# Optimization experiments

Hardware: AMD Instinct MI355X
Metric: run time of the kernel (lower is better)

## Reference

```python
import jax, jax.numpy as jnp
import numpy as np

N = 50000       # population nodes
E = 1_600_000   # edges per edge type
F_IN = 2000     # flattened individual-graph embedding (100*20)
D = 20          # hidden channels per TransformerConv head (heads=1)
NEG_SLOPE = 0.01
BN_EPS = 1e-5


def setup_inputs() -> dict:
    key = jax.random.key(0)
    ks = jax.random.split(key, 24)
    features = jax.random.normal(ks[0], (N, F_IN), jnp.float32)
    same_index = jax.random.randint(ks[1], (2, E), 0, N, dtype=jnp.int64)
    diff_index = jax.random.randint(ks[2], (2, E), 0, N, dtype=jnp.int64)
    s0 = 1.0 / np.sqrt(F_IN)
    s1 = 1.0 / np.sqrt(D)
    # layer 0 conv params, stacked over the 2 edge types (same, diff)
    W0q = jax.random.normal(ks[3], (2, F_IN, D), jnp.float32) * s0
    W0k = jax.random.normal(ks[4], (2, F_IN, D), jnp.float32) * s0
    W0v = jax.random.normal(ks[5], (2, F_IN, D), jnp.float32) * s0
    W0s = jax.random.normal(ks[6], (2, F_IN, D), jnp.float32) * s0
    b0q = jnp.zeros((2, D)); b0k = jnp.zeros((2, D))
    b0v = jnp.zeros((2, D)); b0s = jnp.zeros((2, D))
    # layers 1..3 conv params: [layer, edge_type, D, D]
    Wq = jax.random.normal(ks[7], (3, 2, D, D), jnp.float32) * s1
    Wk = jax.random.normal(ks[8], (3, 2, D, D), jnp.float32) * s1
    Wv = jax.random.normal(ks[9], (3, 2, D, D), jnp.float32) * s1
    Ws = jax.random.normal(ks[10], (3, 2, D, D), jnp.float32) * s1
    bq = jnp.zeros((3, 2, D)); bk = jnp.zeros((3, 2, D))
    bv = jnp.zeros((3, 2, D)); bs = jnp.zeros((3, 2, D))
    w1 = jnp.full((4,), 0.8, jnp.float32)
    w2 = jnp.full((4,), 0.2, jnp.float32)
    bn_gamma = jnp.ones((4, D), jnp.float32)
    bn_beta = jnp.zeros((4, D), jnp.float32)
    Wout = jax.random.normal(ks[11], (4 * D, 2), jnp.float32) / np.sqrt(4 * D)
    bout = jnp.zeros((2,), jnp.float32)
    return dict(features=features, same_index=same_index, diff_index=diff_index,
                W0q=W0q, b0q=b0q, W0k=W0k, b0k=b0k, W0v=W0v, b0v=b0v, W0s=W0s, b0s=b0s,
                Wq=Wq, bq=bq, Wk=Wk, bk=bk, Wv=Wv, bv=bv, Ws=Ws, bs=bs,
                w1=w1, w2=w2, bn_gamma=bn_gamma, bn_beta=bn_beta, Wout=Wout, bout=bout)


def _tconv(x, edge_index, Wq, bq, Wk, bk, Wv, bv, Ws, bs):
    """PyG TransformerConv, heads=1, concat=True, root_weight=True, no edge_attr."""
    src, dst = edge_index[0], edge_index[1]
    q = x @ Wq + bq   # [N, D]
    k = x @ Wk + bk
    v = x @ Wv + bv
    logits = jnp.einsum('ed,ed->e', q[dst], k[src]) / jnp.sqrt(jnp.float32(D))  # [E]
    m = jax.ops.segment_max(logits, dst, num_segments=N)
    m = jnp.where(jnp.isfinite(m), m, jnp.float32(0.0))  # nodes with no in-edges
    e = jnp.exp(logits - m[dst])
    z = jax.ops.segment_sum(e, dst, num_segments=N)
    alpha = e / (z[dst] + 1e-16)  # PyG softmax epsilon
    agg = jax.ops.segment_sum(alpha[:, None] * v[src], dst, num_segments=N)  # [N, D]
    return agg + x @ Ws + bs  # skip (root) connection


def _bn(x, gamma, beta):
    mu = x.mean(axis=0)
    var = x.var(axis=0)
    return (x - mu) * jax.lax.rsqrt(var + BN_EPS) * gamma + beta


def reference(features, same_index, diff_index,
              W0q, b0q, W0k, b0k, W0v, b0v, W0s, b0s,
              Wq, bq, Wk, bk, Wv, bv, Ws, bs,
              w1, w2, bn_gamma, bn_beta, Wout, bout):
    x = features
    fcs = []
    for l in range(4):
        if l == 0:
            p_same = (W0q[0], b0q[0], W0k[0], b0k[0], W0v[0], b0v[0], W0s[0], b0s[0])
            p_diff = (W0q[1], b0q[1], W0k[1], b0k[1], W0v[1], b0v[1], W0s[1], b0s[1])
        else:
            i = l - 1
            p_same = (Wq[i, 0], bq[i, 0], Wk[i, 0], bk[i, 0], Wv[i, 0], bv[i, 0], Ws[i, 0], bs[i, 0])
            p_diff = (Wq[i, 1], bq[i, 1], Wk[i, 1], bk[i, 1], Wv[i, 1], bv[i, 1], Ws[i, 1], bs[i, 1])
        x1 = _tconv(x, same_index, *p_same)
        x2 = _tconv(x, diff_index, *p_diff)
        t = w1[l] + w2[l]
        x = (w1[l] / t) * x1 + (w2[l] / t) * x2
        x = _bn(x, bn_gamma[l], bn_beta[l])
        x = jax.nn.leaky_relu(x, NEG_SLOPE)
        fcs.append(x)
    fc = jnp.concatenate(fcs, axis=-1)  # [N, 80]
    return fc @ Wout + bout  # [N, 2]
```

## Files before the change

kernel.cpp:

```cpp
#include <hip/hip_runtime.h>
#include <math.h>

#define N_NODES 50000
#define E_EDGES 1600000
#define F_IN    2000
#define D       20
#define NCOL    160
#define KPAD    2016
#define NBNP    64

#define INV_SQRT_D 0.22360679774997896f

typedef __bf16 bf16x8 __attribute__((ext_vector_type(8)));
typedef __bf16 bf16x4 __attribute__((ext_vector_type(4)));
typedef float  f32x4  __attribute__((ext_vector_type(4)));


__global__ void pack_kernel(
    const float* __restrict__ W0q, const float* __restrict__ W0k,
    const float* __restrict__ W0v, const float* __restrict__ W0s,
    const float* __restrict__ b0q, const float* __restrict__ b0k,
    const float* __restrict__ b0v, const float* __restrict__ b0s,
    const float* __restrict__ Wq,  const float* __restrict__ Wk,
    const float* __restrict__ Wv,  const float* __restrict__ Ws_,
    const float* __restrict__ bq,  const float* __restrict__ bk,
    const float* __restrict__ bv,  const float* __restrict__ bs_,
    __bf16* __restrict__ B0, float* __restrict__ bias0,
    float* __restrict__ WL, float* __restrict__ biasL,
    float* __restrict__ bnp, int* __restrict__ deg)
{
  long idx = (long)blockIdx.x * blockDim.x + threadIdx.x;
  if (idx < (long)NCOL*KPAD) {
    int col = (int)(idx / KPAD), k = (int)(idx % KPAD);
    int et = col / 80, r = col % 80, mat = r / 20, d = r % 20;
    const float* w = (mat==0)?W0q:(mat==1)?W0s:(mat==2)?W0k:W0v;
    float v = (k < F_IN) ? w[((size_t)et*F_IN + k)*D + d] : 0.f;
    B0[idx] = (__bf16)v;
    return;
  }
  idx -= (long)NCOL*KPAD;
  if (idx < 160) {
    int col = (int)idx;
    int et = col / 80, r = col % 80, mat = r / 20, d = r % 20;
    const float* b = (mat==0)?b0q:(mat==1)?b0s:(mat==2)?b0k:b0v;
    bias0[col] = b[et*D + d];
    return;
  }
  idx -= 160;
  if (idx < 9600) {
    int l = (int)(idx / 3200), rem = (int)(idx % 3200);
    int k = rem / NCOL, col = rem % NCOL;
    int et = col / 80, r = col % 80, mat = r / 20, d = r % 20;
    const float* w = (mat==0)?Wq:(mat==1)?Ws_:(mat==2)?Wk:Wv;
    WL[idx] = w[(((size_t)l*2 + et)*D + k)*D + d];
    return;
  }
  idx -= 9600;
  if (idx < 480) {
    int l = (int)(idx / NCOL), col = (int)(idx % NCOL);
    int et = col / 80, r = col % 80, mat = r / 20, d = r % 20;
    const float* b = (mat==0)?bq:(mat==1)?bs_:(mat==2)?bk:bv;
    biasL[idx] = b[(l*2 + et)*D + d];
    return;
  }
  idx -= 480;
  if (idx < 4*NBNP*40) { bnp[idx] = 0.f; return; }
  idx -= 4*NBNP*40;
  if (idx < 2*N_NODES) { deg[idx] = 0; return; }
}

__global__ void hist_kernel(const int* __restrict__ same, const int* __restrict__ diff,
                            int* __restrict__ deg)
{
  long i = (long)blockIdx.x * blockDim.x + threadIdx.x;
  if (i >= 2L*E_EDGES) return;
  int et = (i >= E_EDGES) ? 1 : 0;
  long e = i - (long)et*E_EDGES;
  const int* ix = et ? diff : same;
  int dst = ix[E_EDGES + e];
  atomicAdd(&deg[(size_t)et*N_NODES + dst], 1);
}

__global__ void scan_kernel(const int* __restrict__ deg,
                            int* __restrict__ rowptr0, int* __restrict__ rowptr1,
                            int* __restrict__ next0, int* __restrict__ next1)
{
  const int et = blockIdx.x;
  const int* dg = deg + (size_t)et*N_NODES;
  int* rp = et ? rowptr1 : rowptr0;
  int* np = et ? next1 : next0;
  __shared__ int part[1024];
  const int t = threadIdx.x;
  const int per = (N_NODES + 1023) / 1024;
  const int b = t * per;
  const int e = (b + per < N_NODES) ? (b + per) : N_NODES;
  int s = 0;
  for (int i = b; i < e; i++) s += dg[i];
  part[t] = s;
  __syncthreads();
  for (int o = 1; o < 1024; o <<= 1) {
    int v = (t >= o) ? part[t-o] : 0;
    __syncthreads();
    part[t] += v;
    __syncthreads();
  }
  int run = (t == 0) ? 0 : part[t-1];
  for (int i = b; i < e; i++) {
    rp[i] = run; np[i] = run;
    run += dg[i];
  }
  if (t == 0) rp[N_NODES] = part[1023];
}

#define SC_EPT 16
#define SC_CHUNK (256*SC_EPT)
__global__ void scatter_kernel(const int* __restrict__ same, const int* __restrict__ diff,
                               int* __restrict__ next0, int* __restrict__ next1,
                               int* __restrict__ adj0, int* __restrict__ adj1)
{
  const int part  = blockIdx.x & 7;
  const int chunk = blockIdx.x >> 3;
  const int lo = part * (N_NODES/8);
  const int hi = lo + (N_NODES/8);
  const long i0 = (long)chunk * SC_CHUNK + threadIdx.x;
#pragma unroll
  for (int it = 0; it < SC_EPT; ++it) {
    long i = i0 + (long)it*256;
    if (i >= 2L*E_EDGES) break;
    int et = (i >= E_EDGES) ? 1 : 0;
    long e = i - (long)et*E_EDGES;
    const int* ix = et ? diff : same;
    int dst = ix[E_EDGES + e];
    if (dst >= lo && dst < hi) {
      int src = ix[e];
      int* np  = et ? next1 : next0;
      int* adj = et ? adj1  : adj0;
      int pos = atomicAdd(&np[dst], 1);
      adj[pos] = src;
    }
  }
}

__launch_bounds__(512)
__global__ void gemm0_mfma(const float* __restrict__ A,
                           const __bf16* __restrict__ Bt,
                           const float* __restrict__ bias,
                           __bf16* __restrict__ QS,
                           __bf16* __restrict__ KV0, __bf16* __restrict__ KV1)
{
  __shared__ __bf16 as[128*32];
  const int t    = threadIdx.x;
  const int lane = t & 63;
  const int wid  = t >> 6;
  const int wr   = wid >> 1;
  const int wc   = wid & 1;
  const int rb0  = blockIdx.x * 128;

  const int srow = t >> 2;
  const int skc  = (t & 3) * 8;
  const int arow = rb0 + srow;
  const float* aptr = A + (size_t)arow * F_IN;

  const int lrow = lane & 15;
  const int lkb  = (lane >> 4) * 8;

  f32x4 acc[2][5];
#pragma unroll
  for (int i = 0; i < 2; i++)
#pragma unroll
    for (int j = 0; j < 5; j++) acc[i][j] = (f32x4){0.f,0.f,0.f,0.f};

  float4 p0, p1;
  auto loadA = [&](int k0) {
    int k = k0 + skc;
    if (arow < N_NODES) {
      if (k + 8 <= F_IN) {
        p0 = *(const float4*)(aptr + k);
        p1 = *(const float4*)(aptr + k + 4);
      } else {
        float tmp[8];
#pragma unroll
        for (int i = 0; i < 8; i++) tmp[i] = (k + i < F_IN) ? aptr[k + i] : 0.f;
        p0 = make_float4(tmp[0],tmp[1],tmp[2],tmp[3]);
        p1 = make_float4(tmp[4],tmp[5],tmp[6],tmp[7]);
      }
    } else {
      p0 = make_float4(0,0,0,0); p1 = p0;
    }
  };

  loadA(0);
  for (int s = 0; s < 63; s++) {
    bf16x8 h;
    h[0]=(__bf16)p0.x; h[1]=(__bf16)p0.y; h[2]=(__bf16)p0.z; h[3]=(__bf16)p0.w;
    h[4]=(__bf16)p1.x; h[5]=(__bf16)p1.y; h[6]=(__bf16)p1.z; h[7]=(__bf16)p1.w;
    *(bf16x8*)&as[srow*32 + skc] = h;
    __syncthreads();
    if (s + 1 < 63) loadA((s + 1) * 32);

    bf16x8 af[2];
#pragma unroll
    for (int rf = 0; rf < 2; rf++)
      af[rf] = *(bf16x8*)&as[(wr*32 + rf*16 + lrow)*32 + lkb];
    bf16x8 bfr[5];
#pragma unroll
    for (int cf = 0; cf < 5; cf++)
      bfr[cf] = *(const bf16x8*)(Bt + (size_t)(wc*80 + cf*16 + lrow)*KPAD + s*32 + lkb);
#pragma unroll
    for (int rf = 0; rf < 2; rf++)
#pragma unroll
      for (int cf = 0; cf < 5; cf++)
        acc[rf][cf] = __builtin_amdgcn_mfma_f32_16x16x32_bf16(af[rf], bfr[cf], acc[rf][cf], 0, 0, 0);
    __syncthreads();
  }

#pragma unroll
  for (int rf = 0; rf < 2; rf++) {
#pragma unroll
    for (int cf = 0; cf < 5; cf++) {
      int col = wc*80 + cf*16 + lrow;
      int et = col / 80, r = col % 80, mat = r / 20, d = r % 20;
      float bv = bias[col];
      __bf16* kvp = et ? KV1 : KV0;
#pragma unroll
      for (int j = 0; j < 4; j++) {
        int row = rb0 + wr*32 + rf*16 + (lane >> 4)*4 + j;
        if (row < N_NODES) {
          __bf16 val = (__bf16)(acc[rf][cf][j] + bv);
          if (mat < 2) QS[(size_t)row*80 + et*40 + mat*20 + d] = val;
          else         kvp[(size_t)row*64 + (mat-2)*20 + d]   = val;
        }
      }
    }
  }
}

__launch_bounds__(256)
__global__ void proj_small_kernel(const float* __restrict__ xp, const float* __restrict__ bnl,
                                  const float* __restrict__ gam, const float* __restrict__ bet,
                                  const float* __restrict__ W, const float* __restrict__ bias,
                                  __bf16* __restrict__ QS,
                                  __bf16* __restrict__ KV0, __bf16* __restrict__ KV1)
{
  __shared__ float ws[20*160];
  __shared__ float xs[16*20];
  __shared__ float Ac[20], Bc[20];
  const int t = threadIdx.x;
  const int n0 = blockIdx.x * 16;
#pragma unroll
  for (int i = 0; i < 13; i++) {
    int idx = t + i*256;
    if (idx < 3200) ws[idx] = W[idx];
  }
  if (t < 20) {
    float s1 = 0.f, s2 = 0.f;
    for (int s = 0; s < NBNP; s++) { s1 += bnl[s*40 + t]; s2 += bnl[s*40 + 20 + t]; }
    float mu  = s1 * (1.f/N_NODES);
    float var = s2 * (1.f/N_NODES) - mu*mu;
    float a = rsqrtf(var + 1e-5f) * gam[t];
    Ac[t] = a; Bc[t] = bet[t] - mu*a;
  }
  __syncthreads();
#pragma unroll
  for (int i = 0; i < 2; i++) {
    int idx = t + i*256;
    if (idx < 320) {
      int nl = idx / 20, k = idx % 20;
      int n = n0 + nl;
      float x = (n < N_NODES) ? xp[(size_t)n*D + k] : 0.f;
      float y = x*Ac[k] + Bc[k];
      xs[idx] = (y > 0.f) ? y : 0.01f*y;
    }
  }
  __syncthreads();
#pragma unroll
  for (int i = 0; i < 10; i++) {
    int idx = t + i*256;
    int nl = idx / NCOL, col = idx % NCOL;
    int n = n0 + nl;
    if (n < N_NODES) {
      float acc = bias[col];
#pragma unroll
      for (int k = 0; k < 20; k++) acc += xs[nl*20 + k] * ws[k*NCOL + col];
      int et = col / 80, r = col % 80, mat = r / 20, d = r % 20;
      __bf16 val = (__bf16)acc;
      if (mat < 2) QS[(size_t)n*80 + et*40 + mat*20 + d] = val;
      else         (et ? KV1 : KV0)[(size_t)n*64 + (mat-2)*20 + d] = val;
    }
  }
}

__launch_bounds__(256)
__global__ void attn_fused(const int* __restrict__ rp0, const int* __restrict__ adj0,
                           const int* __restrict__ rp1, const int* __restrict__ adj1,
                           const __bf16* __restrict__ QS,
                           const __bf16* __restrict__ KV0, const __bf16* __restrict__ KV1,
                           const float* __restrict__ w1, const float* __restrict__ w2, int l,
                           float* __restrict__ xpre, float* __restrict__ bnp)
{
  __shared__ float xnode[4][20];
  const int t    = threadIdx.x;
  const int wv   = t >> 6;
  const int lane = t & 63;
  const int half = lane >> 5;
  const int sl   = lane & 31;
  const int node = blockIdx.x*4 + wv;

  const int* rowptr = half ? rp1 : rp0;
  const int* adj    = half ? adj1 : adj0;
  const __bf16* kvb = half ? KV1 : KV0;
  const __bf16* rq  = QS + (size_t)node*80 + half*40;

  float qf[20];
  {
    bf16x8 q0 = *(const bf16x8*)(rq);
    bf16x8 q1 = *(const bf16x8*)(rq + 8);
    bf16x4 q2 = *(const bf16x4*)(rq + 16);
#pragma unroll
    for (int i = 0; i < 8; i++) { qf[i] = (float)q0[i]; qf[8+i] = (float)q1[i]; }
#pragma unroll
    for (int i = 0; i < 4; i++) qf[16+i] = (float)q2[i];
  }

  const int beg = rowptr[node], end = rowptr[node+1];
  float z = 0.f;
  float S[20];
#pragma unroll
  for (int d = 0; d < 20; d++) S[d] = 0.f;

  for (int i = beg + sl; i < end; i += 32) {
    const int src = adj[i];
    const __bf16* kv = kvb + (size_t)src*64;
    bf16x8 a0 = *(const bf16x8*)(kv);
    bf16x8 a1 = *(const bf16x8*)(kv + 8);
    bf16x8 a2 = *(const bf16x8*)(kv + 16);
    bf16x8 a3 = *(const bf16x8*)(kv + 24);
    bf16x8 a4 = *(const bf16x8*)(kv + 32);
    float d0 = 0.f;
#pragma unroll
    for (int j = 0; j < 8; j++) d0 += qf[j]     * (float)a0[j];
#pragma unroll
    for (int j = 0; j < 8; j++) d0 += qf[8 + j] * (float)a1[j];
#pragma unroll
    for (int j = 0; j < 4; j++) d0 += qf[16 + j]* (float)a2[j];
    const float w0 = __expf(fminf(d0*INV_SQRT_D, 80.f));
    z += w0;
#pragma unroll
    for (int d = 0; d < 4; d++) S[d]     += w0*(float)a2[4+d];
#pragma unroll
    for (int d = 0; d < 8; d++) S[4+d]   += w0*(float)a3[d];
#pragma unroll
    for (int d = 0; d < 8; d++) S[12+d]  += w0*(float)a4[d];
  }

#pragma unroll
  for (int o = 16; o >= 1; o >>= 1) {
    z += __shfl_xor(z, o, 64);
#pragma unroll
    for (int d = 0; d < 20; d++) S[d] += __shfl_xor(S[d], o, 64);
  }

  const float inv = (z > 0.f) ? 1.f/z : 0.f;
  float outv[20];
  {
    bf16x4 s0 = *(const bf16x4*)(rq + 20);
    bf16x8 s1 = *(const bf16x8*)(rq + 24);
    bf16x8 s2 = *(const bf16x8*)(rq + 32);
#pragma unroll
    for (int i = 0; i < 4; i++) outv[i] = S[i]*inv + (float)s0[i];
#pragma unroll
    for (int i = 0; i < 8; i++) { outv[4+i]  = S[4+i]*inv  + (float)s1[i];
                                  outv[12+i] = S[12+i]*inv + (float)s2[i]; }
  }

  const float wa = w1[l], wb = w2[l];
  const float c0 = wa/(wa+wb), c1 = wb/(wa+wb);
  const float cme = half ? c1 : c0;
  const float cot = half ? c0 : c1;
  float x[20];
#pragma unroll
  for (int d = 0; d < 20; d++) {
    float o2 = __shfl_xor(outv[d], 32, 64);
    x[d] = cme*outv[d] + cot*o2;
  }

  if (lane == 0) {
    float* xo = xpre + (size_t)node*D;
#pragma unroll
    for (int j = 0; j < 5; j++) {
      float4 o4 = make_float4(x[4*j], x[4*j+1], x[4*j+2], x[4*j+3]);
      *(float4*)(xo + 4*j) = o4;
    }
#pragma unroll
    for (int d = 0; d < 20; d++) xnode[wv][d] = x[d];
  }
  __syncthreads();

  if (t < 20) {
    float s1 = xnode[0][t] + xnode[1][t] + xnode[2][t] + xnode[3][t];
    float s2 = xnode[0][t]*xnode[0][t] + xnode[1][t]*xnode[1][t]
             + xnode[2][t]*xnode[2][t] + xnode[3][t]*xnode[3][t];
    float* slot = bnp + (blockIdx.x & (NBNP-1))*40;
    atomicAdd(&slot[t], s1);
    atomicAdd(&slot[20 + t], s2);
  }
}

__launch_bounds__(256)
__global__ void final_kernel(const float* __restrict__ xpre4, const float* __restrict__ bnp,
                             const float* __restrict__ gam, const float* __restrict__ bet,
                             const float* __restrict__ Wout, const float* __restrict__ bout,
                             float* __restrict__ out)
{
  __shared__ float Ac[80], Bc[80], wlds[160];
  const int t = threadIdx.x;
  if (t < 80) {
    int l = t / 20, d = t % 20;
    const float* b = bnp + l*(NBNP*40);
    float s1 = 0.f, s2 = 0.f;
    for (int s = 0; s < NBNP; s++) { s1 += b[s*40 + d]; s2 += b[s*40 + 20 + d]; }
    float mu  = s1 * (1.f/N_NODES);
    float var = s2 * (1.f/N_NODES) - mu*mu;
    float a = rsqrtf(var + 1e-5f) * gam[t];
    Ac[t] = a; Bc[t] = bet[t] - mu*a;
  }
  if (t < 160) wlds[t] = Wout[t];
  __syncthreads();

  const int n = blockIdx.x*256 + t;
  if (n >= N_NODES) return;
  float a0 = bout[0], a1 = bout[1];
#pragma unroll
  for (int l = 0; l < 4; l++) {
    const float* base = xpre4 + (size_t)l*N_NODES*D + (size_t)n*D;
#pragma unroll
    for (int d = 0; d < D; d++) {
      int idx = l*20 + d;
      float y = base[d]*Ac[idx] + Bc[idx];
      y = (y > 0.f) ? y : 0.01f*y;
      a0 += y * wlds[idx*2 + 0];
      a1 += y * wlds[idx*2 + 1];
    }
  }
  out[n*2+0] = a0;
  out[n*2+1] = a1;
}

extern "C" void kernel_launch(void* const* d_in, const int* in_sizes, int n_in,
                              void* d_out, int out_size, void* d_ws, size_t ws_size,
                              hipStream_t stream)
{
  const float* feat = (const float*)d_in[0];
  const int*   same = (const int*)d_in[1];
  const int*   diff = (const int*)d_in[2];
  const float* W0q = (const float*)d_in[3];
  const float* b0q = (const float*)d_in[4];
  const float* W0k = (const float*)d_in[5];
  const float* b0k = (const float*)d_in[6];
  const float* W0v = (const float*)d_in[7];
  const float* b0v = (const float*)d_in[8];
  const float* W0s = (const float*)d_in[9];
  const float* b0s = (const float*)d_in[10];
  const float* Wq  = (const float*)d_in[11];
  const float* bq  = (const float*)d_in[12];
  const float* Wk  = (const float*)d_in[13];
  const float* bk  = (const float*)d_in[14];
  const float* Wv  = (const float*)d_in[15];
  const float* bv  = (const float*)d_in[16];
  const float* Ws_ = (const float*)d_in[17];
  const float* bs_ = (const float*)d_in[18];
  const float* w1  = (const float*)d_in[19];
  const float* w2  = (const float*)d_in[20];
  const float* gamma = (const float*)d_in[21];
  const float* beta  = (const float*)d_in[22];
  const float* Wout  = (const float*)d_in[23];
  const float* bout  = (const float*)d_in[24];

  float* wsf  = (float*)d_ws;
  __bf16*  QS    = (__bf16*)wsf;
  __bf16*  KV0   = (__bf16*)(wsf + 2000000);
  __bf16*  KV1   = (__bf16*)(wsf + 3600000);
  float*   XPRE4 = wsf + 5200000;
  __bf16*  B0bf  = (__bf16*)(wsf + 9200000);
  float*   BIAS0 = wsf + 9361280;
  float*   WL    = wsf + 9361440;
  float*   BIASL = wsf + 9371040;
  float*   BNP   = wsf + 9371520;
  int*     ib    = (int*)(wsf + 9381760);
  int* DEG  = ib;
  int* RP0  = ib + 100000;
  int* RP1  = ib + 150004;
  int* NX0  = ib + 200008;
  int* NX1  = ib + 250008;
  int* ADJ0 = ib + 300008;
  int* ADJ1 = ib + 1900008;

  const int packN = NCOL*KPAD + 160 + 9600 + 480 + 4*NBNP*40 + 2*N_NODES;
  pack_kernel<<<(packN + 255)/256, 256, 0, stream>>>(
      W0q, W0k, W0v, W0s, b0q, b0k, b0v, b0s,
      Wq, Wk, Wv, Ws_, bq, bk, bv, bs_,
      B0bf, BIAS0, WL, BIASL, BNP, DEG);

  hist_kernel<<<(2*E_EDGES + 255)/256, 256, 0, stream>>>(same, diff, DEG);
  scan_kernel<<<2, 1024, 0, stream>>>(DEG, RP0, RP1, NX0, NX1);
  {
    const long nchunk = (2L*E_EDGES + SC_CHUNK - 1) / SC_CHUNK;
    scatter_kernel<<<(int)(nchunk*8), 256, 0, stream>>>(same, diff, NX0, NX1, ADJ0, ADJ1);
  }

  for (int l = 0; l < 4; l++) {
    if (l == 0)
      gemm0_mfma<<<(N_NODES + 127)/128, 512, 0, stream>>>(feat, B0bf, BIAS0, QS, KV0, KV1);
    else
      proj_small_kernel<<<(N_NODES + 15)/16, 256, 0, stream>>>(
          XPRE4 + (size_t)(l-1)*N_NODES*D, BNP + (l-1)*(NBNP*40),
          gamma + (l-1)*D, beta + (l-1)*D,
          WL + (size_t)(l-1)*3200, BIASL + (size_t)(l-1)*160, QS, KV0, KV1);

    attn_fused<<<N_NODES/4, 256, 0, stream>>>(
        RP0, ADJ0, RP1, ADJ1, QS, KV0, KV1, w1, w2, l,
        XPRE4 + (size_t)l*N_NODES*D, BNP + l*(NBNP*40));
  }

  final_kernel<<<(N_NODES + 255)/256, 256, 0, stream>>>(
      XPRE4, BNP, gamma, beta, Wout, bout, (float*)d_out);
}
```

Baseline: 986.9 us.

## Fuse GEMM, projection, attention and final layers into one cooperative persistent kernel

Replaces the per-layer sequence of gemm0, proj_small, attn_fused and final kernels with a single cooperative persistent kernel that uses grid.sync between stages. The goal is to remove launch overhead and the inter-kernel drains. The layer-0 GEMM now uses 64-row tiles with 256 threads. BN partial sums are atomically accumulated per node-lane instead of per block via shared memory, and hist_kernel is partitioned by destination range like scatter. The trade-offs are grid-wide barrier costs, reduced occupancy from a fixed grid size, and more atomic traffic on the BN slots.

```diff
diff --git a/kernel.cpp b/kernel.cpp
--- a/kernel.cpp
+++ b/kernel.cpp
@@ -1,5 +1,8 @@
 #include <hip/hip_runtime.h>
+#include <hip/hip_cooperative_groups.h>
 #include <math.h>
+
+namespace cg = cooperative_groups;
 
 #define N_NODES 50000
 #define E_EDGES 1600000
@@ -14,7 +17,6 @@
 typedef __bf16 bf16x8 __attribute__((ext_vector_type(8)));
 typedef __bf16 bf16x4 __attribute__((ext_vector_type(4)));
 typedef float  f32x4  __attribute__((ext_vector_type(4)));
-
 
 __global__ void pack_kernel(
     const float* __restrict__ W0q, const float* __restrict__ W0k,
@@ -69,16 +71,28 @@
   if (idx < 2*N_NODES) { deg[idx] = 0; return; }
 }
 
+#define SC_EPT 16
+#define SC_CHUNK (256*SC_EPT)
+
 __global__ void hist_kernel(const int* __restrict__ same, const int* __restrict__ diff,
                             int* __restrict__ deg)
 {
-  long i = (long)blockIdx.x * blockDim.x + threadIdx.x;
-  if (i >= 2L*E_EDGES) return;
-  int et = (i >= E_EDGES) ? 1 : 0;
-  long e = i - (long)et*E_EDGES;
-  const int* ix = et ? diff : same;
-  int dst = ix[E_EDGES + e];
-  atomicAdd(&deg[(size_t)et*N_NODES + dst], 1);
+  const int part  = blockIdx.x & 7;
+  const int chunk = blockIdx.x >> 3;
+  const int lo = part * (N_NODES/8);
+  const int hi = lo + (N_NODES/8);
+  const long i0 = (long)chunk * SC_CHUNK + threadIdx.x;
+#pragma unroll
+  for (int it = 0; it < SC_EPT; ++it) {
+    long i = i0 + (long)it*256;
+    if (i >= 2L*E_EDGES) break;
+    int et = (i >= E_EDGES) ? 1 : 0;
+    long e = i - (long)et*E_EDGES;
+    const int* ix = et ? diff : same;
+    int dst = ix[E_EDGES + e];
+    if (dst >= lo && dst < hi)
+      atomicAdd(&deg[(size_t)et*N_NODES + dst], 1);
+  }
 }
 
 __global__ void scan_kernel(const int* __restrict__ deg,
@@ -112,8 +126,6 @@
   if (t == 0) rp[N_NODES] = part[1023];
 }
 
-#define SC_EPT 16
-#define SC_CHUNK (256*SC_EPT)
 __global__ void scatter_kernel(const int* __restrict__ same, const int* __restrict__ diff,
                                int* __restrict__ next0, int* __restrict__ next1,
                                int* __restrict__ adj0, int* __restrict__ adj1)
@@ -141,309 +153,313 @@
   }
 }
 
-__launch_bounds__(512)
-__global__ void gemm0_mfma(const float* __restrict__ A,
-                           const __bf16* __restrict__ Bt,
-                           const float* __restrict__ bias,
-                           __bf16* __restrict__ QS,
-                           __bf16* __restrict__ KV0, __bf16* __restrict__ KV1)
+struct MegaP {
+  const float* feat; const __bf16* B0; const float* bias0;
+  const float* WL; const float* biasL;
+  const float* w1; const float* w2; const float* gamma; const float* beta;
+  const float* Wout; const float* bout;
+  const int* rp0; const int* adj0; const int* rp1; const int* adj1;
+  __bf16* QS; __bf16* KV0; __bf16* KV1;
+  float* xpre4; float* bnp; float* out;
+};
+
+__launch_bounds__(256, 4)
+__global__ void mega_kernel(MegaP P)
 {
-  __shared__ __bf16 as[128*32];
+  cg::grid_group grid = cg::this_grid();
+  __shared__ __align__(16) char smem[14336];
   const int t    = threadIdx.x;
+  const int nblk = gridDim.x;
   const int lane = t & 63;
-  const int wid  = t >> 6;
-  const int wr   = wid >> 1;
-  const int wc   = wid & 1;
-  const int rb0  = blockIdx.x * 128;
-
-  const int srow = t >> 2;
-  const int skc  = (t & 3) * 8;
-  const int arow = rb0 + srow;
-  const float* aptr = A + (size_t)arow * F_IN;
-
-  const int lrow = lane & 15;
-  const int lkb  = (lane >> 4) * 8;
-
-  f32x4 acc[2][5];
-#pragma unroll
-  for (int i = 0; i < 2; i++)
-#pragma unroll
-    for (int j = 0; j < 5; j++) acc[i][j] = (f32x4){0.f,0.f,0.f,0.f};
-
-  float4 p0, p1;
-  auto loadA = [&](int k0) {
-    int k = k0 + skc;
-    if (arow < N_NODES) {
-      if (k + 8 <= F_IN) {
-        p0 = *(const float4*)(aptr + k);
-        p1 = *(const float4*)(aptr + k + 4);
-      } else {
-        float tmp[8];
-#pragma unroll
-        for (int i = 0; i < 8; i++) tmp[i] = (k + i < F_IN) ? aptr[k + i] : 0.f;
-        p0 = make_float4(tmp[0],tmp[1],tmp[2],tmp[3]);
-        p1 = make_float4(tmp[4],tmp[5],tmp[6],tmp[7]);
-      }
-    } else {
-      p0 = make_float4(0,0,0,0); p1 = p0;
+  const int wv   = t >> 6;
+
+  {
+    __bf16* as = (__bf16*)smem;
+    const int wr   = wv >> 1;
+    const int wc   = wv & 1;
+    const int srow = t >> 2;
+    const int skc  = (t & 3) * 8;
+    const int lrow = lane & 15;
+    const int lkb  = (lane >> 4) * 8;
+
+    for (int tile = blockIdx.x; tile < 782; tile += nblk) {
+      const int rb0  = tile * 64;
+      const int arow = rb0 + srow;
+      const float* aptr = P.feat + (size_t)arow * F_IN;
+
+      f32x4 acc[2][5];
+#pragma unroll
+      for (int i = 0; i < 2; i++)
+#pragma unroll
+        for (int j = 0; j < 5; j++) acc[i][j] = (f32x4){0.f,0.f,0.f,0.f};
+
+      float4 p0, p1;
+      auto loadA = [&](int k0) {
+        int k = k0 + skc;
+        if (arow < N_NODES) {
+          p0 = *(const float4*)(aptr + k);
+          p1 = *(const float4*)(aptr + k + 4);
+        } else {
+          p0 = make_float4(0,0,0,0); p1 = p0;
+        }
+      };
+
+      loadA(0);
+      for (int s = 0; s < 63; s++) {
+        bf16x8 h;
+        h[0]=(__bf16)p0.x; h[1]=(__bf16)p0.y; h[2]=(__bf16)p0.z; h[3]=(__bf16)p0.w;
+        h[4]=(__bf16)p1.x; h[5]=(__bf16)p1.y; h[6]=(__bf16)p1.z; h[7]=(__bf16)p1.w;
+        __syncthreads();
+        *(bf16x8*)&as[srow*32 + skc] = h;
+        __syncthreads();
+        if (s + 1 < 63) loadA((s + 1) * 32);
+
+        bf16x8 af[2];
+#pragma unroll
+        for (int rf = 0; rf < 2; rf++)
+          af[rf] = *(bf16x8*)&as[(wr*32 + rf*16 + lrow)*32 + lkb];
+        bf16x8 bfr[5];
+#pragma unroll
+        for (int cf = 0; cf < 5; cf++)
+          bfr[cf] = *(const bf16x8*)(P.B0 + (size_t)(wc*80 + cf*16 + lrow)*KPAD + s*32 + lkb);
+#pragma unroll
+        for (int rf = 0; rf < 2; rf++)
+#pragma unroll
+          for (int cf = 0; cf < 5; cf++)
+            acc[rf][cf] = __builtin_amdgcn_mfma_f32_16x16x32_bf16(af[rf], bfr[cf], acc[rf][cf], 0, 0, 0);
+      }
+
+#pragma unroll
+      for (int rf = 0; rf < 2; rf++) {
+#pragma unroll
+        for (int cf = 0; cf < 5; cf++) {
+          int col = wc*80 + cf*16 + lrow;
+          int et = col / 80, r = col % 80, mat = r / 20, d = r % 20;
+          float bv = P.bias0[col];
+          __bf16* kvp = et ? P.KV1 : P.KV0;
+#pragma unroll
+          for (int j = 0; j < 4; j++) {
+            int row = rb0 + wr*32 + rf*16 + (lane >> 4)*4 + j;
+            if (row < N_NODES) {
+              __bf16 val = (__bf16)(acc[rf][cf][j] + bv);
+              if (mat < 2) P.QS[(size_t)row*80 + et*40 + mat*20 + d] = val;
+              else         kvp[(size_t)row*64 + (mat-2)*20 + d]     = val;
+            }
+          }
+        }
+      }
     }
-  };
-
-  loadA(0);
-  for (int s = 0; s < 63; s++) {
-    bf16x8 h;
-    h[0]=(__bf16)p0.x; h[1]=(__bf16)p0.y; h[2]=(__bf16)p0.z; h[3]=(__bf16)p0.w;
-    h[4]=(__bf16)p1.x; h[5]=(__bf16)p1.y; h[6]=(__bf16)p1.z; h[7]=(__bf16)p1.w;
-    *(bf16x8*)&as[srow*32 + skc] = h;
+  }
+  grid.sync();
+
+  for (int l = 0; l < 4; ++l) {
+    if (l > 0) {
+      float* ws = (float*)smem;
+      float* xs = (float*)smem + 3200;
+      float* Ac = (float*)smem + 3520;
+      float* Bc = (float*)smem + 3540;
+      const float* bnl  = P.bnp + (size_t)(l-1)*(NBNP*40);
+      const float* W    = P.WL + (size_t)(l-1)*3200;
+      const float* bias = P.biasL + (size_t)(l-1)*160;
+      const float* xp   = P.xpre4 + (size_t)(l-1)*N_NODES*D;
+
+      __syncthreads();
+#pragma unroll
+      for (int i = 0; i < 13; i++) {
+        int idx = t + i*256;
+        if (idx < 3200) ws[idx] = W[idx];
+      }
+      if (t < 20) {
+        float s1 = 0.f, s2 = 0.f;
+        for (int s = 0; s < NBNP; s++) { s1 += bnl[s*40 + t]; s2 += bnl[s*40 + 20 + t]; }
+        float mu  = s1 * (1.f/N_NODES);
+        float var = s2 * (1.f/N_NODES) - mu*mu;
+        float a = rsqrtf(var + 1e-5f) * P.gamma[(l-1)*D + t];
+        Ac[t] = a; Bc[t] = P.beta[(l-1)*D + t] - mu*a;
+      }
+      __syncthreads();
+
+      for (int tile = blockIdx.x; tile < 3125; tile += nblk) {
+        const int n0 = tile * 16;
+        __syncthreads();
+#pragma unroll
+        for (int i = 0; i < 2; i++) {
+          int idx = t + i*256;
+          if (idx < 320) {
+            int nl = idx / 20, k = idx % 20;
+            int n = n0 + nl;
+            float x = (n < N_NODES) ? xp[(size_t)n*D + k] : 0.f;
+            float y = x*Ac[k] + Bc[k];
+            xs[idx] = (y > 0.f) ? y : 0.01f*y;
+          }
+        }
+        __syncthreads();
+#pragma unroll
+        for (int i = 0; i < 10; i++) {
+          int idx = t + i*256;
+          int nl = idx / NCOL, col = idx % NCOL;
+          int n = n0 + nl;
+          if (n < N_NODES) {
+            float acc = bias[col];
+#pragma unroll
+            for (int k = 0; k < 20; k++) acc += xs[nl*20 + k] * ws[k*NCOL + col];
+            int et = col / 80, r = col % 80, mat = r / 20, d = r % 20;
+            __bf16 val = (__bf16)acc;
+            if (mat < 2) P.QS[(size_t)n*80 + et*40 + mat*20 + d] = val;
+            else         (et ? P.KV1 : P.KV0)[(size_t)n*64 + (mat-2)*20 + d] = val;
+          }
+        }
+      }
+      grid.sync();
+    }
+
+    {
+      const int half = lane >> 5;
+      const int sl   = lane & 31;
+      const int* rowptr = half ? P.rp1 : P.rp0;
+      const int* adj    = half ? P.adj1 : P.adj0;
+      const __bf16* kvb = half ? P.KV1 : P.KV0;
+      const float wa = P.w1[l], wb = P.w2[l];
+      const float c0 = wa/(wa+wb), c1 = wb/(wa+wb);
+      const float cme = half ? c1 : c0;
+      const float cot = half ? c0 : c1;
+      float* xpre = P.xpre4 + (size_t)l*N_NODES*D;
+      float* bnpl = P.bnp + (size_t)l*(NBNP*40);
+
+      for (int g = blockIdx.x; g < 12500; g += nblk) {
+        const int node = g*4 + wv;
+        const __bf16* rq = P.QS + (size_t)node*80 + half*40;
+
+        float qf[20];
+        {
+          bf16x8 q0 = *(const bf16x8*)(rq);
+          bf16x8 q1 = *(const bf16x8*)(rq + 8);
+          bf16x4 q2 = *(const bf16x4*)(rq + 16);
+#pragma unroll
+          for (int i = 0; i < 8; i++) { qf[i] = (float)q0[i]; qf[8+i] = (float)q1[i]; }
+#pragma unroll
+          for (int i = 0; i < 4; i++) qf[16+i] = (float)q2[i];
+        }
+
+        const int beg = rowptr[node], end = rowptr[node+1];
+        float z = 0.f;
+        float S[20];
+#pragma unroll
+        for (int d = 0; d < 20; d++) S[d] = 0.f;
+
+        for (int i = beg + sl; i < end; i += 32) {
+          const int src = adj[i];
+          const __bf16* kv = kvb + (size_t)src*64;
+          bf16x8 a0 = *(const bf16x8*)(kv);
+          bf16x8 a1 = *(const bf16x8*)(kv + 8);
+          bf16x8 a2 = *(const bf16x8*)(kv + 16);
+          bf16x8 a3 = *(const bf16x8*)(kv + 24);
+          bf16x8 a4 = *(const bf16x8*)(kv + 32);
+          float d0 = 0.f;
+#pragma unroll
+          for (int j = 0; j < 8; j++) d0 += qf[j]     * (float)a0[j];
+#pragma unroll
+          for (int j = 0; j < 8; j++) d0 += qf[8 + j] * (float)a1[j];
+#pragma unroll
+          for (int j = 0; j < 4; j++) d0 += qf[16 + j]* (float)a2[j];
+          const float w0 = __expf(fminf(d0*INV_SQRT_D, 80.f));
+          z += w0;
+#pragma unroll
+          for (int d = 0; d < 4; d++) S[d]     += w0*(float)a2[4+d];
+#pragma unroll
+          for (int d = 0; d < 8; d++) S[4+d]   += w0*(float)a3[d];
+#pragma unroll
+          for (int d = 0; d < 8; d++) S[12+d]  += w0*(float)a4[d];
+        }
+
+#pragma unroll
+        for (int o = 16; o >= 1; o >>= 1) {
+          z += __shfl_xor(z, o, 64);
+#pragma unroll
+          for (int d = 0; d < 20; d++) S[d] += __shfl_xor(S[d], o, 64);
+        }
+
+        const float inv = (z > 0.f) ? 1.f/z : 0.f;
+        float outv[20];
+        {
+          bf16x4 s0 = *(const bf16x4*)(rq + 20);
+          bf16x8 s1 = *(const bf16x8*)(rq + 24);
+          bf16x8 s2 = *(const bf16x8*)(rq + 32);
+#pragma unroll
+          for (int i2 = 0; i2 < 4; i2++) outv[i2] = S[i2]*inv + (float)s0[i2];
+#pragma unroll
+          for (int i2 = 0; i2 < 8; i2++) { outv[4+i2]  = S[4+i2]*inv  + (float)s1[i2];
+                                           outv[12+i2] = S[12+i2]*inv + (float)s2[i2]; }
+        }
+
+        float x[20];
+#pragma unroll
+        for (int d = 0; d < 20; d++) {
+          float o2 = __shfl_xor(outv[d], 32, 64);
+          x[d] = cme*outv[d] + cot*o2;
+        }
+
+        if (lane == 0) {
+          float* xo = xpre + (size_t)node*D;
+#pragma unroll
+          for (int j = 0; j < 5; j++) {
+            float4 o4 = make_float4(x[4*j], x[4*j+1], x[4*j+2], x[4*j+3]);
+            *(float4*)(xo + 4*j) = o4;
+          }
+        }
+
+        float v = x[0];
+#pragma unroll
+        for (int d = 1; d < 20; d++) v = (sl == d) ? x[d] : v;
+        if (sl < 20) {
+          float* slot = bnpl + (size_t)(node & (NBNP-1))*40;
+          if (half == 0) atomicAdd(&slot[sl], v);
+          else           atomicAdd(&slot[20 + sl], v*v);
+        }
+      }
+    }
+    grid.sync();
+  }
+
+  {
+    float* Ac   = (float*)smem;
+    float* Bc   = (float*)smem + 80;
+    float* wlds = (float*)smem + 160;
     __syncthreads();
-    if (s + 1 < 63) loadA((s + 1) * 32);
-
-    bf16x8 af[2];
-#pragma unroll
-    for (int rf = 0; rf < 2; rf++)
-      af[rf] = *(bf16x8*)&as[(wr*32 + rf*16 + lrow)*32 + lkb];
-    bf16x8 bfr[5];
-#pragma unroll
-    for (int cf = 0; cf < 5; cf++)
-      bfr[cf] = *(const bf16x8*)(Bt + (size_t)(wc*80 + cf*16 + lrow)*KPAD + s*32 + lkb);
-#pragma unroll
-    for (int rf = 0; rf < 2; rf++)
-#pragma unroll
-      for (int cf = 0; cf < 5; cf++)
-        acc[rf][cf] = __builtin_amdgcn_mfma_f32_16x16x32_bf16(af[rf], bfr[cf], acc[rf][cf], 0, 0, 0);
+    if (t < 80) {
+      int l = t / 20, d = t % 20;
+      const float* b = P.bnp + (size_t)l*(NBNP*40);
+      float s1 = 0.f, s2 = 0.f;
+      for (int s = 0; s < NBNP; s++) { s1 += b[s*40 + d]; s2 += b[s*40 + 20 + d]; }
+      float mu  = s1 * (1.f/N_NODES);
+      float var = s2 * (1.f/N_NODES) - mu*mu;
+      float a = rsqrtf(var + 1e-5f) * P.gamma[t];
+      Ac[t] = a; Bc[t] = P.beta[t] - mu*a;
+    }
+    if (t < 160) wlds[t] = P.Wout[t];
     __syncthreads();
-  }
-
-#pragma unroll
-  for (int rf = 0; rf < 2; rf++) {
-#pragma unroll
-    for (int cf = 0; cf < 5; cf++) {
-      int col = wc*80 + cf*16 + lrow;
-      int et = col / 80, r = col % 80, mat = r / 20, d = r % 20;
-      float bv = bias[col];
-      __bf16* kvp = et ? KV1 : KV0;
-#pragma unroll
-      for (int j = 0; j < 4; j++) {
-        int row = rb0 + wr*32 + rf*16 + (lane >> 4)*4 + j;
-        if (row < N_NODES) {
-          __bf16 val = (__bf16)(acc[rf][cf][j] + bv);
-          if (mat < 2) QS[(size_t)row*80 + et*40 + mat*20 + d] = val;
-          else         kvp[(size_t)row*64 + (mat-2)*20 + d]   = val;
-        }
-      }
+
+    const float b0 = P.bout[0], b1 = P.bout[1];
+    for (int tile = blockIdx.x; tile < 196; tile += nblk) {
+      const int n = tile*256 + t;
+      if (n >= N_NODES) continue;
+      float a0 = b0, a1 = b1;
+#pragma unroll
+      for (int l = 0; l < 4; l++) {
+        const float* base = P.xpre4 + (size_t)l*N_NODES*D + (size_t)n*D;
+#pragma unroll
+        for (int d = 0; d < D; d++) {
+          int idx = l*20 + d;
+          float y = base[d]*Ac[idx] + Bc[idx];
+          y = (y > 0.f) ? y : 0.01f*y;
+          a0 += y * wlds[idx*2 + 0];
+          a1 += y * wlds[idx*2 + 1];
+        }
+      }
+      P.out[n*2+0] = a0;
+      P.out[n*2+1] = a1;
     }
   }
-}
-
-__launch_bounds__(256)
-__global__ void proj_small_kernel(const float* __restrict__ xp, const float* __restrict__ bnl,
-                                  const float* __restrict__ gam, const float* __restrict__ bet,
-                                  const float* __restrict__ W, const float* __restrict__ bias,
-                                  __bf16* __restrict__ QS,
-                                  __bf16* __restrict__ KV0, __bf16* __restrict__ KV1)
-{
-  __shared__ float ws[20*160];
-  __shared__ float xs[16*20];
-  __shared__ float Ac[20], Bc[20];
-  const int t = threadIdx.x;
-  const int n0 = blockIdx.x * 16;
-#pragma unroll
-  for (int i = 0; i < 13; i++) {
-    int idx = t + i*256;
-    if (idx < 3200) ws[idx] = W[idx];
-  }
-  if (t < 20) {
-    float s1 = 0.f, s2 = 0.f;
-    for (int s = 0; s < NBNP; s++) { s1 += bnl[s*40 + t]; s2 += bnl[s*40 + 20 + t]; }
-    float mu  = s1 * (1.f/N_NODES);
-    float var = s2 * (1.f/N_NODES) - mu*mu;
-    float a = rsqrtf(var + 1e-5f) * gam[t];
-    Ac[t] = a; Bc[t] = bet[t] - mu*a;
-  }
-  __syncthreads();
-#pragma unroll
-  for (int i = 0; i < 2; i++) {
-    int idx = t + i*256;
-    if (idx < 320) {
-      int nl = idx / 20, k = idx % 20;
-      int n = n0 + nl;
-      float x = (n < N_NODES) ? xp[(size_t)n*D + k] : 0.f;
-      float y = x*Ac[k] + Bc[k];
-      xs[idx] = (y > 0.f) ? y : 0.01f*y;
-    }
-  }
-  __syncthreads();
-#pragma unroll
-  for (int i = 0; i < 10; i++) {
-    int idx = t + i*256;
-    int nl = idx / NCOL, col = idx % NCOL;
-    int n = n0 + nl;
-    if (n < N_NODES) {
-      float acc = bias[col];
-#pragma unroll
-      for (int k = 0; k < 20; k++) acc += xs[nl*20 + k] * ws[k*NCOL + col];
-      int et = col / 80, r = col % 80, mat = r / 20, d = r % 20;
-      __bf16 val = (__bf16)acc;
-      if (mat < 2) QS[(size_t)n*80 + et*40 + mat*20 + d] = val;
-      else         (et ? KV1 : KV0)[(size_t)n*64 + (mat-2)*20 + d] = val;
-    }
-  }
-}
-
-__launch_bounds__(256)
-__global__ void attn_fused(const int* __restrict__ rp0, const int* __restrict__ adj0,
-                           const int* __restrict__ rp1, const int* __restrict__ adj1,
-                           const __bf16* __restrict__ QS,
-                           const __bf16* __restrict__ KV0, const __bf16* __restrict__ KV1,
-                           const float* __restrict__ w1, const float* __restrict__ w2, int l,
-                           float* __restrict__ xpre, float* __restrict__ bnp)
-{
-  __shared__ float xnode[4][20];
-  const int t    = threadIdx.x;
-  const int wv   = t >> 6;
-  const int lane = t & 63;
-  const int half = lane >> 5;
-  const int sl   = lane & 31;
-  const int node = blockIdx.x*4 + wv;
-
-  const int* rowptr = half ? rp1 : rp0;
-  const int* adj    = half ? adj1 : adj0;
-  const __bf16* kvb = half ? KV1 : KV0;
-  const __bf16* rq  = QS + (size_t)node*80 + half*40;
-
-  float qf[20];
-  {
-    bf16x8 q0 = *(const bf16x8*)(rq);
-    bf16x8 q1 = *(const bf16x8*)(rq + 8);
-    bf16x4 q2 = *(const bf16x4*)(rq + 16);
-#pragma unroll
-    for (int i = 0; i < 8; i++) { qf[i] = (float)q0[i]; qf[8+i] = (float)q1[i]; }
-#pragma unroll
-    for (int i = 0; i < 4; i++) qf[16+i] = (float)q2[i];
-  }
-
-  const int beg = rowptr[node], end = rowptr[node+1];
-  float z = 0.f;
-  float S[20];
-#pragma unroll
-  for (int d = 0; d < 20; d++) S[d] = 0.f;
-
-  for (int i = beg + sl; i < end; i += 32) {
-    const int src = adj[i];
-    const __bf16* kv = kvb + (size_t)src*64;
-    bf16x8 a0 = *(const bf16x8*)(kv);
-    bf16x8 a1 = *(const bf16x8*)(kv + 8);
-    bf16x8 a2 = *(const bf16x8*)(kv + 16);
-    bf16x8 a3 = *(const bf16x8*)(kv + 24);
-    bf16x8 a4 = *(const bf16x8*)(kv + 32);
-    float d0 = 0.f;
-#pragma unroll
-    for (int j = 0; j < 8; j++) d0 += qf[j]     * (float)a0[j];
-#pragma unroll
-    for (int j = 0; j < 8; j++) d0 += qf[8 + j] * (float)a1[j];
-#pragma unroll
-    for (int j = 0; j < 4; j++) d0 += qf[16 + j]* (float)a2[j];
-    const float w0 = __expf(fminf(d0*INV_SQRT_D, 80.f));
-    z += w0;
-#pragma unroll
-    for (int d = 0; d < 4; d++) S[d]     += w0*(float)a2[4+d];
-#pragma unroll
-    for (int d = 0; d < 8; d++) S[4+d]   += w0*(float)a3[d];
-#pragma unroll
-    for (int d = 0; d < 8; d++) S[12+d]  += w0*(float)a4[d];
-  }
-
-#pragma unroll
-  for (int o = 16; o >= 1; o >>= 1) {
-    z += __shfl_xor(z, o, 64);
-#pragma unroll
-    for (int d = 0; d < 20; d++) S[d] += __shfl_xor(S[d], o, 64);
-  }
-
-  const float inv = (z > 0.f) ? 1.f/z : 0.f;
-  float outv[20];
-  {
-    bf16x4 s0 = *(const bf16x4*)(rq + 20);
-    bf16x8 s1 = *(const bf16x8*)(rq + 24);
-    bf16x8 s2 = *(const bf16x8*)(rq + 32);
-#pragma unroll
-    for (int i = 0; i < 4; i++) outv[i] = S[i]*inv + (float)s0[i];
-#pragma unroll
-    for (int i = 0; i < 8; i++) { outv[4+i]  = S[4+i]*inv  + (float)s1[i];
-                                  outv[12+i] = S[12+i]*inv + (float)s2[i]; }
-  }
-
-  const float wa = w1[l], wb = w2[l];
-  const float c0 = wa/(wa+wb), c1 = wb/(wa+wb);
-  const float cme = half ? c1 : c0;
-  const float cot = half ? c0 : c1;
-  float x[20];
-#pragma unroll
-  for (int d = 0; d < 20; d++) {
-    float o2 = __shfl_xor(outv[d], 32, 64);
-    x[d] = cme*outv[d] + cot*o2;
-  }
-
-  if (lane == 0) {
-    float* xo = xpre + (size_t)node*D;
-#pragma unroll
-    for (int j = 0; j < 5; j++) {
-      float4 o4 = make_float4(x[4*j], x[4*j+1], x[4*j+2], x[4*j+3]);
-      *(float4*)(xo + 4*j) = o4;
-    }
-#pragma unroll
-    for (int d = 0; d < 20; d++) xnode[wv][d] = x[d];
-  }
-  __syncthreads();
-
-  if (t < 20) {
-    float s1 = xnode[0][t] + xnode[1][t] + xnode[2][t] + xnode[3][t];
-    float s2 = xnode[0][t]*xnode[0][t] + xnode[1][t]*xnode[1][t]
-             + xnode[2][t]*xnode[2][t] + xnode[3][t]*xnode[3][t];
-    float* slot = bnp + (blockIdx.x & (NBNP-1))*40;
-    atomicAdd(&slot[t], s1);
-    atomicAdd(&slot[20 + t], s2);
-  }
-}
-
-__launch_bounds__(256)
-__global__ void final_kernel(const float* __restrict__ xpre4, const float* __restrict__ bnp,
-                             const float* __restrict__ gam, const float* __restrict__ bet,
-                             const float* __restrict__ Wout, const float* __restrict__ bout,
-                             float* __restrict__ out)
-{
-  __shared__ float Ac[80], Bc[80], wlds[160];
-  const int t = threadIdx.x;
-  if (t < 80) {
-    int l = t / 20, d = t % 20;
-    const float* b = bnp + l*(NBNP*40);
-    float s1 = 0.f, s2 = 0.f;
-    for (int s = 0; s < NBNP; s++) { s1 += b[s*40 + d]; s2 += b[s*40 + 20 + d]; }
-    float mu  = s1 * (1.f/N_NODES);
-    float var = s2 * (1.f/N_NODES) - mu*mu;
-    float a = rsqrtf(var + 1e-5f) * gam[t];
-    Ac[t] = a; Bc[t] = bet[t] - mu*a;
-  }
-  if (t < 160) wlds[t] = Wout[t];
-  __syncthreads();
-
-  const int n = blockIdx.x*256 + t;
-  if (n >= N_NODES) return;
-  float a0 = bout[0], a1 = bout[1];
-#pragma unroll
-  for (int l = 0; l < 4; l++) {
-    const float* base = xpre4 + (size_t)l*N_NODES*D + (size_t)n*D;
-#pragma unroll
-    for (int d = 0; d < D; d++) {
-      int idx = l*20 + d;
-      float y = base[d]*Ac[idx] + Bc[idx];
-      y = (y > 0.f) ? y : 0.01f*y;
-      a0 += y * wlds[idx*2 + 0];
-      a1 += y * wlds[idx*2 + 1];
-    }
-  }
-  out[n*2+0] = a0;
-  out[n*2+1] = a1;
 }
 
 extern "C" void kernel_launch(void* const* d_in, const int* in_sizes, int n_in,
@@ -501,27 +517,27 @@
       Wq, Wk, Wv, Ws_, bq, bk, bv, bs_,
       B0bf, BIAS0, WL, BIASL, BNP, DEG);
 
-  hist_kernel<<<(2*E_EDGES + 255)/256, 256, 0, stream>>>(same, diff, DEG);
+  const long nchunk = (2L*E_EDGES + SC_CHUNK - 1) / SC_CHUNK;
+  hist_kernel<<<(int)(nchunk*8), 256, 0, stream>>>(same, diff, DEG);
   scan_kernel<<<2, 1024, 0, stream>>>(DEG, RP0, RP1, NX0, NX1);
-  {
-    const long nchunk = (2L*E_EDGES + SC_CHUNK - 1) / SC_CHUNK;
-    scatter_kernel<<<(int)(nchunk*8), 256, 0, stream>>>(same, diff, NX0, NX1, ADJ0, ADJ1);
-  }
-
-  for (int l = 0; l < 4; l++) {
-    if (l == 0)
-      gemm0_mfma<<<(N_NODES + 127)/128, 512, 0, stream>>>(feat, B0bf, BIAS0, QS, KV0, KV1);
-    else
-      proj_small_kernel<<<(N_NODES + 15)/16, 256, 0, stream>>>(
-          XPRE4 + (size_t)(l-1)*N_NODES*D, BNP + (l-1)*(NBNP*40),
-          gamma + (l-1)*D, beta + (l-1)*D,
-          WL + (size_t)(l-1)*3200, BIASL + (size_t)(l-1)*160, QS, KV0, KV1);
-
-    attn_fused<<<N_NODES/4, 256, 0, stream>>>(
-        RP0, ADJ0, RP1, ADJ1, QS, KV0, KV1, w1, w2, l,
-        XPRE4 + (size_t)l*N_NODES*D, BNP + l*(NBNP*40));
-  }
-
-  final_kernel<<<(N_NODES + 255)/256, 256, 0, stream>>>(
-      XPRE4, BNP, gamma, beta, Wout, bout, (float*)d_out);
+  scatter_kernel<<<(int)(nchunk*8), 256, 0, stream>>>(same, diff, NX0, NX1, ADJ0, ADJ1);
+
+  MegaP P;
+  P.feat = feat; P.B0 = B0bf; P.bias0 = BIAS0;
+  P.WL = WL; P.biasL = BIASL;
+  P.w1 = w1; P.w2 = w2; P.gamma = gamma; P.beta = beta;
+  P.Wout = Wout; P.bout = bout;
+  P.rp0 = RP0; P.adj0 = ADJ0; P.rp1 = RP1; P.adj1 = ADJ1;
+  P.QS = QS; P.KV0 = KV0; P.KV1 = KV1;
+  P.xpre4 = XPRE4; P.bnp = BNP; P.out = (float*)d_out;
+
+  int nb = 0;
+  if (hipOccupancyMaxActiveBlocksPerMultiprocessor(&nb, (const void*)mega_kernel, 256, 0)
+      != hipSuccess || nb < 1) nb = 2;
+  if (nb > 8) nb = 8;
+  int gridsz = nb * 256;
+
+  void* kargs[] = { &P };
+  hipLaunchCooperativeKernel((const void*)mega_kernel, dim3(gridsz), dim3(256),
+                             kargs, 0, stream);
 }
```

New measurement: 1.810 ms. 1.83x slower.
